# Kernel tuning notes

Hardware: AMD Instinct MI355X
Metric: run time of the kernel (lower is better)

## Reference

```python
import jax, jax.numpy as jnp
import numpy as np

R, B, D, C = 64, 4096, 512, 128  # n_rules, batch, n_fea, n_cls


def setup_inputs() -> dict:
    key = jax.random.key(0)
    k0, k1, k2, k3, k4 = jax.random.split(key, 5)
    x = jax.random.normal(k0, (B, D), dtype=jnp.float32)
    proto = jax.random.normal(k1, (R, D), dtype=jnp.float32)
    var = jax.random.uniform(k2, (R, D), dtype=jnp.float32)
    W = jax.random.normal(k3, (R, D, C), dtype=jnp.float32) * 0.02
    b = jax.random.normal(k4, (R, C), dtype=jnp.float32) * 0.02
    return {"x": x, "proto": proto, "var": var, "W": W, "b": b}


def reference(x, proto, var, W, b):
    # Antecedent: Gaussian membership per rule, var clamped to [1e-4, 0.1]
    v = jnp.clip(var, 0.0001, 0.1)                                  # [R, D]
    diff = x[None, :, :] - proto[:, None, :]                        # [R, B, D]
    m = jnp.exp(-diff * diff / (2.0 * v[:, None, :] ** 2))          # [R, B, D]
    # Firing strength: sum of squared memberships over features, softmax over rules
    fs_ini = jnp.sum(m * m, axis=-1).T                              # [B, R]
    fire_strength = jax.nn.softmax(fs_ini, axis=1)                  # [B, R]
    # Consequent: per-rule Linear + ReLU (batched GEMM over rules)
    expert = jax.nn.relu(jnp.einsum('bd,rdc->rbc', x, W) + b[:, None, :])  # [R, B, C]
    # Softmax-weighted combine over rules
    out = jnp.einsum('rbc,br->bc', expert, fire_strength)           # [B, C]
    return out, fire_strength
```

## Files before the change

### kernel.cpp

```cpp
#include <hip/hip_runtime.h>
#include <hip/hip_bf16.h>
#include <cmath>

#define R_ 64
#define B_ 4096
#define D_ 512
#define C_ 128

typedef __attribute__((ext_vector_type(8))) short bf16x8;
typedef __attribute__((ext_vector_type(4))) float f32x4;

__device__ __forceinline__ unsigned short f2bf(float f) {
  union { float f; unsigned u; } x; x.f = f;
  unsigned r = (x.u + 0x7FFFu + ((x.u >> 16) & 1u)) >> 16;
  return (unsigned short)r;
}

__global__ void prep_x_kernel(const float* __restrict__ x, unsigned short* __restrict__ xw) {
  int i = blockIdx.x * 256 + threadIdx.x;
  float4 v = reinterpret_cast<const float4*>(x)[i];
  ushort4 o;
  o.x = f2bf(v.x); o.y = f2bf(v.y); o.z = f2bf(v.z); o.w = f2bf(v.w);
  reinterpret_cast<ushort4*>(xw)[i] = o;
}

__global__ void prep_w_kernel(const float* __restrict__ W, unsigned short* __restrict__ wt) {
  __shared__ float t[32][33];
  int bx = blockIdx.x;
  int r = bx >> 6;
  int rem = bx & 63;
  int d0 = (rem >> 2) << 5;
  int c0 = (rem & 3) << 5;
  int tx = threadIdx.x & 31, ty = threadIdx.x >> 5;
  const float* Wr = W + (size_t)r * D_ * C_;
#pragma unroll
  for (int q = 0; q < 4; ++q) {
    int dl = q * 8 + ty;
    t[dl][tx] = Wr[(size_t)(d0 + dl) * C_ + c0 + tx];
  }
  __syncthreads();
  unsigned short* wtr = wt + (size_t)r * C_ * D_;
#pragma unroll
  for (int q = 0; q < 4; ++q) {
    int cl = q * 8 + ty;
    float v = t[tx][cl];
    wtr[(size_t)(c0 + cl) * D_ + d0 + tx] = f2bf(v);
  }
}

__global__ void prep_ps_kernel(const float* __restrict__ proto, const float* __restrict__ var,
                               float* __restrict__ ps) {
  int i = blockIdx.x * 256 + threadIdx.x;
  float v = fminf(fmaxf(var[i], 1e-4f), 0.1f);
  float s = 1.2011224087864498f / v;
  float2 o; o.x = s; o.y = -proto[i] * s;
  reinterpret_cast<float2*>(ps)[i] = o;
}

__global__ __launch_bounds__(256, 4) void fs_partial_kernel(
    const float* __restrict__ x, const float* __restrict__ ps,
    float* __restrict__ fire) {
  __shared__ float x_s[16 * 68];
  __shared__ __align__(16) float ps_s[64 * 128];
  const int tid = threadIdx.x;
  const int b0 = blockIdx.x * 16;
  const int dq = blockIdx.y;

  {
    int row = tid >> 4, c4 = tid & 15;
    float4 v = *reinterpret_cast<const float4*>(&x[(size_t)(b0 + row) * D_ + dq * 64 + c4 * 4]);
    *reinterpret_cast<float4*>(&x_s[row * 68 + c4 * 4]) = v;
  }
#pragma unroll
  for (int k = 0; k < 8; ++k) {
    int g = tid + k * 256;
    int row = g >> 5, gi = g & 31;
    float4 v = *reinterpret_cast<const float4*>(&ps[(size_t)row * (D_ * 2) + dq * 128 + gi * 4]);
    int gs = gi ^ (row & 31);
    *reinterpret_cast<float4*>((char*)ps_s + row * 512 + (gs << 4)) = v;
  }
  __syncthreads();

  const int tr = tid & 63;
  const int tb = tid >> 6;
  const int s31 = tr & 31;
  const char* pb = (const char*)ps_s + tr * 512;
  float facc[4] = {0.f, 0.f, 0.f, 0.f};

#pragma unroll
  for (int d4 = 0; d4 < 16; ++d4) {
    float4 psa = *reinterpret_cast<const float4*>(pb + ((((d4 * 2) ^ s31)) << 4));
    float4 psb = *reinterpret_cast<const float4*>(pb + ((((d4 * 2 + 1) ^ s31)) << 4));
#pragma unroll
    for (int i = 0; i < 4; ++i) {
      float4 xv = *reinterpret_cast<const float4*>(&x_s[(tb * 4 + i) * 68 + d4 * 4]);
      float u0 = fmaf(xv.x, psa.x, psa.y);
      float u1 = fmaf(xv.y, psa.z, psa.w);
      float u2 = fmaf(xv.z, psb.x, psb.y);
      float u3 = fmaf(xv.w, psb.z, psb.w);
      facc[i] += exp2f(-(u0 * u0)) + exp2f(-(u1 * u1)) +
                 exp2f(-(u2 * u2)) + exp2f(-(u3 * u3));
    }
  }
#pragma unroll
  for (int i = 0; i < 4; ++i)
    atomicAdd(&fire[(size_t)(b0 + tb * 4 + i) * R_ + tr], facc[i]);
}

__global__ void softmax_kernel(float* __restrict__ fire) {
  const int b = blockIdx.x * 4 + (threadIdx.x >> 6);
  const int r = threadIdx.x & 63;
  float v = fire[(size_t)b * R_ + r];
  float m = v;
#pragma unroll
  for (int off = 32; off; off >>= 1) m = fmaxf(m, __shfl_xor(m, off, 64));
  float e = exp2f((v - m) * 1.4426950408889634f);
  float s = e;
#pragma unroll
  for (int off = 32; off; off >>= 1) s += __shfl_xor(s, off, 64);
  fire[(size_t)b * R_ + r] = e / s;
}

__global__ __launch_bounds__(256, 2) void gemm_kernel(
    const unsigned short* __restrict__ xw, const unsigned short* __restrict__ wt,
    const float* __restrict__ fire, const float* __restrict__ bias,
    float* __restrict__ out) {
  __shared__ __align__(16) unsigned short x_s[2][128 * 64];
  __shared__ __align__(16) unsigned short w_s[2][128 * 64];
  __shared__ float fire_s[128 * 4];
  __shared__ float bias_s[4 * 128];

  const int tid = threadIdx.x;
  const int bm = blockIdx.x;
  const int rg = blockIdx.y;
  const int b0 = bm * 128;

  {
    for (int t = tid; t < 512; t += 256) {
      int row = t >> 2, g = t & 3;
      fire_s[t] = fire[(size_t)(b0 + row) * R_ + rg * 4 + g];
    }
    for (int t = tid; t < 512; t += 256) {
      bias_s[t] = bias[rg * 4 * C_ + t];
    }
  }

  const int wid = tid >> 6, lane = tid & 63;
  const int wm = wid >> 1, wn = wid & 1;
  const int l16 = lane & 15, lhi = lane >> 4;

  int offA[4][2], offB[4][2];
#pragma unroll
  for (int m = 0; m < 4; ++m) {
    int row = wm * 64 + m * 16 + l16;
#pragma unroll
    for (int ks = 0; ks < 2; ++ks)
      offA[m][ks] = row * 128 + (((ks * 4 + lhi) ^ (row & 7)) << 4);
  }
#pragma unroll
  for (int n = 0; n < 4; ++n) {
    int row = wn * 64 + n * 16 + l16;
#pragma unroll
    for (int ks = 0; ks < 2; ++ks)
      offB[n][ks] = row * 128 + (((ks * 4 + lhi) ^ (row & 7)) << 4);
  }

  const unsigned short* xsrc = xw + (size_t)b0 * D_;
  const unsigned short* wbase = wt + (size_t)(rg * 4) * C_ * D_;

  float tot[4][4][4];
#pragma unroll
  for (int m = 0; m < 4; ++m)
#pragma unroll
    for (int n = 0; n < 4; ++n)
#pragma unroll
      for (int j = 0; j < 4; ++j) tot[m][n][j] = 0.f;

  f32x4 acc[4][4];

  auto stage = [&](unsigned short* lds, const unsigned short* src, int kc) {
#pragma unroll
    for (int q = 0; q < 4; ++q) {
      int ch = q * 256 + tid;
      int row = ch >> 3, g = ch & 7;
      const unsigned short* ga = src + (size_t)row * D_ + kc + ((g ^ (row & 7)) << 3);
      __builtin_amdgcn_global_load_lds(
          (const __attribute__((address_space(1))) void*)ga,
          (__attribute__((address_space(3))) void*)(lds + ch * 8), 16, 0, 0);
    }
  };

  stage(x_s[0], xsrc, 0);
  stage(w_s[0], wbase, 0);
  asm volatile("s_waitcnt vmcnt(0)" ::: "memory");
  __syncthreads();

  int cur = 0;
  for (int s = 0; s < 32; ++s) {
    const int g = s >> 3, kk = s & 7;
    if (kk == 0) {
#pragma unroll
      for (int m = 0; m < 4; ++m)
#pragma unroll
        for (int n = 0; n < 4; ++n)
          acc[m][n] = f32x4{0.f, 0.f, 0.f, 0.f};
    }
    if (s + 1 < 32) {
      const int s1 = s + 1;
      stage(x_s[cur ^ 1], xsrc, (s1 & 7) * 64);
      stage(w_s[cur ^ 1], wbase + (size_t)(s1 >> 3) * C_ * D_, (s1 & 7) * 64);
    }
    const char* xb = (const char*)x_s[cur];
    const char* wb = (const char*)w_s[cur];
    bf16x8 av[4][2], bv[4][2];
#pragma unroll
    for (int m = 0; m < 4; ++m)
#pragma unroll
      for (int ks = 0; ks < 2; ++ks)
        av[m][ks] = *reinterpret_cast<const bf16x8*>(xb + offA[m][ks]);
#pragma unroll
    for (int n = 0; n < 4; ++n)
#pragma unroll
      for (int ks = 0; ks < 2; ++ks)
        bv[n][ks] = *reinterpret_cast<const bf16x8*>(wb + offB[n][ks]);
#pragma unroll
    for (int ks = 0; ks < 2; ++ks)
#pragma unroll
      for (int m = 0; m < 4; ++m)
#pragma unroll
        for (int n = 0; n < 4; ++n)
          acc[m][n] = __builtin_amdgcn_mfma_f32_16x16x32_bf16(av[m][ks], bv[n][ks], acc[m][n], 0, 0, 0);
    if (kk == 7) {
#pragma unroll
      for (int m = 0; m < 4; ++m)
#pragma unroll
        for (int n = 0; n < 4; ++n) {
          int col = wn * 64 + n * 16 + l16;
          float bi = bias_s[g * 128 + col];
#pragma unroll
          for (int j = 0; j < 4; ++j) {
            int rowl = wm * 64 + m * 16 + lhi * 4 + j;
            float v = acc[m][n][j] + bi;
            v = fmaxf(v, 0.f);
            tot[m][n][j] += v * fire_s[rowl * 4 + g];
          }
        }
    }
    asm volatile("s_waitcnt vmcnt(0)" ::: "memory");
    __syncthreads();
    cur ^= 1;
  }

#pragma unroll
  for (int m = 0; m < 4; ++m)
#pragma unroll
    for (int n = 0; n < 4; ++n) {
      int col = wn * 64 + n * 16 + l16;
#pragma unroll
      for (int j = 0; j < 4; ++j) {
        int rowl = wm * 64 + m * 16 + lhi * 4 + j;
        atomicAdd(&out[(size_t)(b0 + rowl) * C_ + col], tot[m][n][j]);
      }
    }
}

extern "C" void kernel_launch(void* const* d_in, const int* in_sizes, int n_in,
                              void* d_out, int out_size, void* d_ws, size_t ws_size,
                              hipStream_t stream) {
  const float* x     = (const float*)d_in[0];
  const float* proto = (const float*)d_in[1];
  const float* var   = (const float*)d_in[2];
  const float* W     = (const float*)d_in[3];
  const float* bias  = (const float*)d_in[4];
  float* out  = (float*)d_out;
  float* fire = out + (size_t)B_ * C_;

  const size_t WS_X  = (size_t)B_ * D_ * sizeof(unsigned short);
  const size_t WS_WT = (size_t)R_ * C_ * D_ * sizeof(unsigned short);
  const size_t WS_PS = (size_t)R_ * D_ * 2 * sizeof(float);
  if (ws_size < WS_X + WS_WT + WS_PS) return;

  unsigned short* xw  = (unsigned short*)d_ws;
  unsigned short* wtp = (unsigned short*)((char*)d_ws + WS_X);
  float*          ps  = (float*)((char*)d_ws + WS_X + WS_WT);

  hipMemsetAsync(d_out, 0, (size_t)out_size * sizeof(float), stream);
  prep_x_kernel<<<dim3((B_ * D_ / 4) / 256), dim3(256), 0, stream>>>(x, xw);
  prep_w_kernel<<<dim3(R_ * 64), dim3(256), 0, stream>>>(W, wtp);
  prep_ps_kernel<<<dim3(R_ * D_ / 256), dim3(256), 0, stream>>>(proto, var, ps);
  fs_partial_kernel<<<dim3(B_ / 16, 8), dim3(256), 0, stream>>>(x, ps, fire);
  softmax_kernel<<<dim3(B_ / 4), dim3(256), 0, stream>>>(fire);
  gemm_kernel<<<dim3(B_ / 128, R_ / 4), dim3(256), 0, stream>>>(xw, wtp, fire, bias, out);
}
```

Baseline: 121.3 us.

## Enlarge GEMM tile to 256x128 with 512 threads and triple-buffered prefetch

```diff
diff --git a/kernel.cpp b/kernel.cpp
--- a/kernel.cpp
+++ b/kernel.cpp
@@ -9,6 +9,8 @@
 
 typedef __attribute__((ext_vector_type(8))) short bf16x8;
 typedef __attribute__((ext_vector_type(4))) float f32x4;
+
+#define VMCNT(n) asm volatile("s_waitcnt vmcnt(" #n ")" ::: "memory")
 
 __device__ __forceinline__ unsigned short f2bf(float f) {
   union { float f; unsigned u; } x; x.f = f;
@@ -121,28 +123,28 @@
   fire[(size_t)b * R_ + r] = e / s;
 }
 
-__global__ __launch_bounds__(256, 2) void gemm_kernel(
+__global__ __launch_bounds__(512, 2) void gemm_kernel(
     const unsigned short* __restrict__ xw, const unsigned short* __restrict__ wt,
     const float* __restrict__ fire, const float* __restrict__ bias,
     float* __restrict__ out) {
-  __shared__ __align__(16) unsigned short x_s[2][128 * 64];
-  __shared__ __align__(16) unsigned short w_s[2][128 * 64];
-  __shared__ float fire_s[128 * 4];
+  __shared__ __align__(16) unsigned short x_s[3][256 * 64];
+  __shared__ __align__(16) unsigned short w_s[3][128 * 64];
+  __shared__ float fire_s[256 * 4];
   __shared__ float bias_s[4 * 128];
 
   const int tid = threadIdx.x;
-  const int bm = blockIdx.x;
-  const int rg = blockIdx.y;
-  const int b0 = bm * 128;
+  const int rg = blockIdx.x;
+  const int bm = blockIdx.y;
+  const int b0 = bm * 256;
 
   {
-    for (int t = tid; t < 512; t += 256) {
+#pragma unroll
+    for (int q = 0; q < 2; ++q) {
+      int t = q * 512 + tid;
       int row = t >> 2, g = t & 3;
       fire_s[t] = fire[(size_t)(b0 + row) * R_ + rg * 4 + g];
     }
-    for (int t = tid; t < 512; t += 256) {
-      bias_s[t] = bias[rg * 4 * C_ + t];
-    }
+    bias_s[tid >= 512 ? 0 : tid] = bias[rg * 4 * C_ + tid];
   }
 
   const int wid = tid >> 6, lane = tid & 63;
@@ -165,9 +167,40 @@
       offB[n][ks] = row * 128 + (((ks * 4 + lhi) ^ (row & 7)) << 4);
   }
 
+  int aoff[4], adst[4], boff[2], bdst[2];
+#pragma unroll
+  for (int q = 0; q < 4; ++q) {
+    int ch = q * 512 + tid;
+    int row = ch >> 3, g = ch & 7;
+    aoff[q] = row * D_ + ((g ^ (row & 7)) << 3);
+    adst[q] = ch * 8;
+  }
+#pragma unroll
+  for (int q = 0; q < 2; ++q) {
+    int ch = q * 512 + tid;
+    int row = ch >> 3, g = ch & 7;
+    boff[q] = row * D_ + ((g ^ (row & 7)) << 3);
+    bdst[q] = ch * 8;
+  }
+
   const unsigned short* xsrc = xw + (size_t)b0 * D_;
   const unsigned short* wbase = wt + (size_t)(rg * 4) * C_ * D_;
 
+  auto stageA = [&](unsigned short* lds, const unsigned short* src) {
+#pragma unroll
+    for (int q = 0; q < 4; ++q)
+      __builtin_amdgcn_global_load_lds(
+          (const __attribute__((address_space(1))) void*)(src + aoff[q]),
+          (__attribute__((address_space(3))) void*)(lds + adst[q]), 16, 0, 0);
+  };
+  auto stageB = [&](unsigned short* lds, const unsigned short* src) {
+#pragma unroll
+    for (int q = 0; q < 2; ++q)
+      __builtin_amdgcn_global_load_lds(
+          (const __attribute__((address_space(1))) void*)(src + boff[q]),
+          (__attribute__((address_space(3))) void*)(lds + bdst[q]), 16, 0, 0);
+  };
+
   float tot[4][4][4];
 #pragma unroll
   for (int m = 0; m < 4; ++m)
@@ -178,24 +211,13 @@
 
   f32x4 acc[4][4];
 
-  auto stage = [&](unsigned short* lds, const unsigned short* src, int kc) {
-#pragma unroll
-    for (int q = 0; q < 4; ++q) {
-      int ch = q * 256 + tid;
-      int row = ch >> 3, g = ch & 7;
-      const unsigned short* ga = src + (size_t)row * D_ + kc + ((g ^ (row & 7)) << 3);
-      __builtin_amdgcn_global_load_lds(
-          (const __attribute__((address_space(1))) void*)ga,
-          (__attribute__((address_space(3))) void*)(lds + ch * 8), 16, 0, 0);
-    }
-  };
-
-  stage(x_s[0], xsrc, 0);
-  stage(w_s[0], wbase, 0);
-  asm volatile("s_waitcnt vmcnt(0)" ::: "memory");
-  __syncthreads();
-
-  int cur = 0;
+  stageA(x_s[0], xsrc);
+  stageB(w_s[0], wbase);
+  stageA(x_s[1], xsrc + 64);
+  stageB(w_s[1], wbase + 64);
+  VMCNT(6);
+  __builtin_amdgcn_s_barrier();
+
   for (int s = 0; s < 32; ++s) {
     const int g = s >> 3, kk = s & 7;
     if (kk == 0) {
@@ -205,13 +227,15 @@
         for (int n = 0; n < 4; ++n)
           acc[m][n] = f32x4{0.f, 0.f, 0.f, 0.f};
     }
-    if (s + 1 < 32) {
-      const int s1 = s + 1;
-      stage(x_s[cur ^ 1], xsrc, (s1 & 7) * 64);
-      stage(w_s[cur ^ 1], wbase + (size_t)(s1 >> 3) * C_ * D_, (s1 & 7) * 64);
-    }
-    const char* xb = (const char*)x_s[cur];
-    const char* wb = (const char*)w_s[cur];
+    if (s + 2 < 32) {
+      const int s2 = s + 2;
+      unsigned short* xb2 = x_s[s2 % 3];
+      unsigned short* wb2 = w_s[s2 % 3];
+      stageA(xb2, xsrc + (s2 & 7) * 64);
+      stageB(wb2, wbase + (size_t)(s2 >> 3) * C_ * D_ + (s2 & 7) * 64);
+    }
+    const char* xb = (const char*)x_s[s % 3];
+    const char* wb = (const char*)w_s[s % 3];
     bf16x8 av[4][2], bv[4][2];
 #pragma unroll
     for (int m = 0; m < 4; ++m)
@@ -246,9 +270,9 @@
           }
         }
     }
-    asm volatile("s_waitcnt vmcnt(0)" ::: "memory");
-    __syncthreads();
-    cur ^= 1;
+    if (s < 30) { VMCNT(6); }
+    else if (s == 30) { VMCNT(0); }
+    if (s < 31) __builtin_amdgcn_s_barrier();
   }
 
 #pragma unroll
@@ -290,5 +314,5 @@
   prep_ps_kernel<<<dim3(R_ * D_ / 256), dim3(256), 0, stream>>>(proto, var, ps);
   fs_partial_kernel<<<dim3(B_ / 16, 8), dim3(256), 0, stream>>>(x, ps, fire);
   softmax_kernel<<<dim3(B_ / 4), dim3(256), 0, stream>>>(fire);
-  gemm_kernel<<<dim3(B_ / 128, R_ / 4), dim3(256), 0, stream>>>(xw, wtp, fire, bias, out);
-}
+  gemm_kernel<<<dim3(16, 16), dim3(512), 0, stream>>>(xw, wtp, fire, bias, out);
+}
```

Result: slower. 131.7 us (+8.6%).

## Shrink GEMM block tile, halve K step, and reorder grid for rule-major launch

Applied to the files above, without the earlier changes.

```diff
diff --git a/kernel.cpp b/kernel.cpp
--- a/kernel.cpp
+++ b/kernel.cpp
@@ -121,144 +121,146 @@
   fire[(size_t)b * R_ + r] = e / s;
 }
 
-__global__ __launch_bounds__(256, 2) void gemm_kernel(
+__global__ __launch_bounds__(256, 4) void gemm_kernel(
     const unsigned short* __restrict__ xw, const unsigned short* __restrict__ wt,
     const float* __restrict__ fire, const float* __restrict__ bias,
     float* __restrict__ out) {
-  __shared__ __align__(16) unsigned short x_s[2][128 * 64];
-  __shared__ __align__(16) unsigned short w_s[2][128 * 64];
-  __shared__ float fire_s[128 * 4];
+  __shared__ __align__(16) unsigned short x_s[2][64 * 32];
+  __shared__ __align__(16) unsigned short w_s[2][128 * 32];
+  __shared__ float fire_s[64 * 4];
   __shared__ float bias_s[4 * 128];
 
   const int tid = threadIdx.x;
-  const int bm = blockIdx.x;
-  const int rg = blockIdx.y;
-  const int b0 = bm * 128;
+  const int rg = blockIdx.x;
+  const int bm = blockIdx.y;
+  const int b0 = bm * 64;
 
   {
-    for (int t = tid; t < 512; t += 256) {
-      int row = t >> 2, g = t & 3;
-      fire_s[t] = fire[(size_t)(b0 + row) * R_ + rg * 4 + g];
-    }
-    for (int t = tid; t < 512; t += 256) {
-      bias_s[t] = bias[rg * 4 * C_ + t];
-    }
+    int row = tid >> 2, g = tid & 3;
+    fire_s[tid] = fire[(size_t)(b0 + row) * R_ + rg * 4 + g];
+    bias_s[tid] = bias[rg * 4 * C_ + tid];
+    bias_s[tid + 256] = bias[rg * 4 * C_ + tid + 256];
   }
 
   const int wid = tid >> 6, lane = tid & 63;
   const int wm = wid >> 1, wn = wid & 1;
   const int l16 = lane & 15, lhi = lane >> 4;
 
-  int offA[4][2], offB[4][2];
-#pragma unroll
-  for (int m = 0; m < 4; ++m) {
-    int row = wm * 64 + m * 16 + l16;
-#pragma unroll
-    for (int ks = 0; ks < 2; ++ks)
-      offA[m][ks] = row * 128 + (((ks * 4 + lhi) ^ (row & 7)) << 4);
+  int offA[2], offB[4];
+#pragma unroll
+  for (int m = 0; m < 2; ++m) {
+    int row = wm * 32 + m * 16 + l16;
+    offA[m] = row * 64 + ((lhi ^ (row & 3)) << 4);
   }
 #pragma unroll
   for (int n = 0; n < 4; ++n) {
     int row = wn * 64 + n * 16 + l16;
-#pragma unroll
-    for (int ks = 0; ks < 2; ++ks)
-      offB[n][ks] = row * 128 + (((ks * 4 + lhi) ^ (row & 7)) << 4);
+    offB[n] = row * 64 + ((lhi ^ (row & 3)) << 4);
+  }
+
+  int a_off, a_dst;
+  {
+    int ch = tid;
+    int row = ch >> 2, g4 = ch & 3;
+    a_off = row * D_ + ((g4 ^ (row & 3)) << 3);
+    a_dst = ch * 8;
+  }
+  int b_off[2], b_dst[2];
+#pragma unroll
+  for (int q = 0; q < 2; ++q) {
+    int ch = q * 256 + tid;
+    int row = ch >> 2, g4 = ch & 3;
+    b_off[q] = row * D_ + ((g4 ^ (row & 3)) << 3);
+    b_dst[q] = ch * 8;
   }
 
   const unsigned short* xsrc = xw + (size_t)b0 * D_;
   const unsigned short* wbase = wt + (size_t)(rg * 4) * C_ * D_;
 
-  float tot[4][4][4];
-#pragma unroll
-  for (int m = 0; m < 4; ++m)
+  auto stageA = [&](unsigned short* lds, int kc) {
+    __builtin_amdgcn_global_load_lds(
+        (const __attribute__((address_space(1))) void*)(xsrc + a_off + kc),
+        (__attribute__((address_space(3))) void*)(lds + a_dst), 16, 0, 0);
+  };
+  auto stageB = [&](unsigned short* lds, const unsigned short* src, int kc) {
+#pragma unroll
+    for (int q = 0; q < 2; ++q)
+      __builtin_amdgcn_global_load_lds(
+          (const __attribute__((address_space(1))) void*)(src + b_off[q] + kc),
+          (__attribute__((address_space(3))) void*)(lds + b_dst[q]), 16, 0, 0);
+  };
+
+  float tot[2][4][4];
+#pragma unroll
+  for (int m = 0; m < 2; ++m)
 #pragma unroll
     for (int n = 0; n < 4; ++n)
 #pragma unroll
       for (int j = 0; j < 4; ++j) tot[m][n][j] = 0.f;
 
-  f32x4 acc[4][4];
-
-  auto stage = [&](unsigned short* lds, const unsigned short* src, int kc) {
-#pragma unroll
-    for (int q = 0; q < 4; ++q) {
-      int ch = q * 256 + tid;
-      int row = ch >> 3, g = ch & 7;
-      const unsigned short* ga = src + (size_t)row * D_ + kc + ((g ^ (row & 7)) << 3);
-      __builtin_amdgcn_global_load_lds(
-          (const __attribute__((address_space(1))) void*)ga,
-          (__attribute__((address_space(3))) void*)(lds + ch * 8), 16, 0, 0);
-    }
-  };
-
-  stage(x_s[0], xsrc, 0);
-  stage(w_s[0], wbase, 0);
-  asm volatile("s_waitcnt vmcnt(0)" ::: "memory");
+  f32x4 acc[2][4];
+
+  stageA(x_s[0], 0);
+  stageB(w_s[0], wbase, 0);
   __syncthreads();
 
   int cur = 0;
-  for (int s = 0; s < 32; ++s) {
-    const int g = s >> 3, kk = s & 7;
+  for (int s = 0; s < 64; ++s) {
+    const int g = s >> 4, kk = s & 15;
     if (kk == 0) {
 #pragma unroll
-      for (int m = 0; m < 4; ++m)
+      for (int m = 0; m < 2; ++m)
 #pragma unroll
         for (int n = 0; n < 4; ++n)
           acc[m][n] = f32x4{0.f, 0.f, 0.f, 0.f};
     }
-    if (s + 1 < 32) {
+    if (s + 1 < 64) {
       const int s1 = s + 1;
-      stage(x_s[cur ^ 1], xsrc, (s1 & 7) * 64);
-      stage(w_s[cur ^ 1], wbase + (size_t)(s1 >> 3) * C_ * D_, (s1 & 7) * 64);
+      stageA(x_s[cur ^ 1], (s1 & 15) * 32);
+      stageB(w_s[cur ^ 1], wbase + (size_t)(s1 >> 4) * C_ * D_, (s1 & 15) * 32);
     }
     const char* xb = (const char*)x_s[cur];
     const char* wb = (const char*)w_s[cur];
-    bf16x8 av[4][2], bv[4][2];
-#pragma unroll
-    for (int m = 0; m < 4; ++m)
-#pragma unroll
-      for (int ks = 0; ks < 2; ++ks)
-        av[m][ks] = *reinterpret_cast<const bf16x8*>(xb + offA[m][ks]);
+    bf16x8 av[2], bv[4];
+#pragma unroll
+    for (int m = 0; m < 2; ++m)
+      av[m] = *reinterpret_cast<const bf16x8*>(xb + offA[m]);
 #pragma unroll
     for (int n = 0; n < 4; ++n)
-#pragma unroll
-      for (int ks = 0; ks < 2; ++ks)
-        bv[n][ks] = *reinterpret_cast<const bf16x8*>(wb + offB[n][ks]);
-#pragma unroll
-    for (int ks = 0; ks < 2; ++ks)
-#pragma unroll
-      for (int m = 0; m < 4; ++m)
-#pragma unroll
-        for (int n = 0; n < 4; ++n)
-          acc[m][n] = __builtin_amdgcn_mfma_f32_16x16x32_bf16(av[m][ks], bv[n][ks], acc[m][n], 0, 0, 0);
-    if (kk == 7) {
-#pragma unroll
-      for (int m = 0; m < 4; ++m)
+      bv[n] = *reinterpret_cast<const bf16x8*>(wb + offB[n]);
+#pragma unroll
+    for (int m = 0; m < 2; ++m)
+#pragma unroll
+      for (int n = 0; n < 4; ++n)
+        acc[m][n] = __builtin_amdgcn_mfma_f32_16x16x32_bf16(av[m], bv[n], acc[m][n], 0, 0, 0);
+    if (kk == 15) {
+#pragma unroll
+      for (int m = 0; m < 2; ++m)
 #pragma unroll
         for (int n = 0; n < 4; ++n) {
           int col = wn * 64 + n * 16 + l16;
           float bi = bias_s[g * 128 + col];
 #pragma unroll
           for (int j = 0; j < 4; ++j) {
-            int rowl = wm * 64 + m * 16 + lhi * 4 + j;
+            int rowl = wm * 32 + m * 16 + lhi * 4 + j;
             float v = acc[m][n][j] + bi;
             v = fmaxf(v, 0.f);
             tot[m][n][j] += v * fire_s[rowl * 4 + g];
           }
         }
     }
-    asm volatile("s_waitcnt vmcnt(0)" ::: "memory");
     __syncthreads();
     cur ^= 1;
   }
 
 #pragma unroll
-  for (int m = 0; m < 4; ++m)
+  for (int m = 0; m < 2; ++m)
 #pragma unroll
     for (int n = 0; n < 4; ++n) {
       int col = wn * 64 + n * 16 + l16;
 #pragma unroll
       for (int j = 0; j < 4; ++j) {
-        int rowl = wm * 64 + m * 16 + lhi * 4 + j;
+        int rowl = wm * 32 + m * 16 + lhi * 4 + j;
         atomicAdd(&out[(size_t)(b0 + rowl) * C_ + col], tot[m][n][j]);
       }
     }
@@ -290,5 +292,5 @@
   prep_ps_kernel<<<dim3(R_ * D_ / 256), dim3(256), 0, stream>>>(proto, var, ps);
   fs_partial_kernel<<<dim3(B_ / 16, 8), dim3(256), 0, stream>>>(x, ps, fire);
   softmax_kernel<<<dim3(B_ / 4), dim3(256), 0, stream>>>(fire);
-  gemm_kernel<<<dim3(B_ / 128, R_ / 4), dim3(256), 0, stream>>>(xw, wtp, fire, bias, out);
-}
+  gemm_kernel<<<dim3(16, 64), dim3(256), 0, stream>>>(xw, wtp, fire, bias, out);
+}
```

New measurement: 129.3 us (median of 3 runs). 1.07x slower.

## Pre-pack x and W into MFMA fragment layout and drop LDS staging in GEMM

Applied to the files above, without the earlier changes.

```diff
diff --git a/kernel.cpp b/kernel.cpp
--- a/kernel.cpp
+++ b/kernel.cpp
@@ -16,35 +16,56 @@
   return (unsigned short)r;
 }
 
-__global__ void prep_x_kernel(const float* __restrict__ x, unsigned short* __restrict__ xw) {
-  int i = blockIdx.x * 256 + threadIdx.x;
-  float4 v = reinterpret_cast<const float4*>(x)[i];
-  ushort4 o;
-  o.x = f2bf(v.x); o.y = f2bf(v.y); o.z = f2bf(v.z); o.w = f2bf(v.w);
-  reinterpret_cast<ushort4*>(xw)[i] = o;
-}
-
-__global__ void prep_w_kernel(const float* __restrict__ W, unsigned short* __restrict__ wt) {
-  __shared__ float t[32][33];
-  int bx = blockIdx.x;
-  int r = bx >> 6;
-  int rem = bx & 63;
-  int d0 = (rem >> 2) << 5;
-  int c0 = (rem & 3) << 5;
-  int tx = threadIdx.x & 31, ty = threadIdx.x >> 5;
-  const float* Wr = W + (size_t)r * D_ * C_;
-#pragma unroll
-  for (int q = 0; q < 4; ++q) {
-    int dl = q * 8 + ty;
-    t[dl][tx] = Wr[(size_t)(d0 + dl) * C_ + c0 + tx];
+__global__ __launch_bounds__(256) void prep_xf_kernel(const float* __restrict__ x,
+                                                      unsigned short* __restrict__ xf) {
+  __shared__ float s[16][516];
+  const int mt = blockIdx.x;
+  const int t = threadIdx.x;
+#pragma unroll
+  for (int p = 0; p < 8; ++p) {
+    int idx = p * 256 + t;
+    int row = idx >> 7, c4 = idx & 127;
+    float4 v = *reinterpret_cast<const float4*>(&x[(size_t)(mt * 16 + row) * D_ + c4 * 4]);
+    *reinterpret_cast<float4*>(&s[row][c4 * 4]) = v;
   }
   __syncthreads();
-  unsigned short* wtr = wt + (size_t)r * C_ * D_;
-#pragma unroll
-  for (int q = 0; q < 4; ++q) {
-    int cl = q * 8 + ty;
-    float v = t[tx][cl];
-    wtr[(size_t)(c0 + cl) * D_ + d0 + tx] = f2bf(v);
+  const int lane = t & 63, l16 = lane & 15, lhi = lane >> 4;
+#pragma unroll
+  for (int p = 0; p < 4; ++p) {
+    int kc = (t >> 6) + p * 4;
+    const float* src = &s[l16][kc * 32 + lhi * 8];
+    unsigned short o[8];
+#pragma unroll
+    for (int e = 0; e < 8; ++e) o[e] = f2bf(src[e]);
+    *reinterpret_cast<bf16x8*>(xf + ((size_t)(mt * 16 + kc)) * 512 + lane * 8) =
+        *reinterpret_cast<bf16x8*>(o);
+  }
+}
+
+__global__ __launch_bounds__(256) void prep_wf_kernel(const float* __restrict__ W,
+                                                      unsigned short* __restrict__ wf) {
+  __shared__ float s[32][132];
+  const int kc = blockIdx.x;
+  const int r = blockIdx.y;
+  const int t = threadIdx.x;
+#pragma unroll
+  for (int p = 0; p < 4; ++p) {
+    int idx = p * 256 + t;
+    int row = idx >> 5, c4 = idx & 31;
+    float4 v = *reinterpret_cast<const float4*>(
+        &W[((size_t)r * D_ + kc * 32 + row) * C_ + c4 * 4]);
+    *reinterpret_cast<float4*>(&s[row][c4 * 4]) = v;
+  }
+  __syncthreads();
+  const int lane = t & 63, l16 = lane & 15, lhi = lane >> 4;
+#pragma unroll
+  for (int p = 0; p < 2; ++p) {
+    int nt = (t >> 6) + p * 4;
+    unsigned short o[8];
+#pragma unroll
+    for (int e = 0; e < 8; ++e) o[e] = f2bf(s[lhi * 8 + e][nt * 16 + l16]);
+    *reinterpret_cast<bf16x8*>(wf + ((size_t)((r * 8 + nt) * 16 + kc)) * 512 + lane * 8) =
+        *reinterpret_cast<bf16x8*>(o);
   }
 }
 
@@ -122,51 +143,29 @@
 }
 
 __global__ __launch_bounds__(256, 2) void gemm_kernel(
-    const unsigned short* __restrict__ xw, const unsigned short* __restrict__ wt,
+    const unsigned short* __restrict__ xf, const unsigned short* __restrict__ wf,
     const float* __restrict__ fire, const float* __restrict__ bias,
     float* __restrict__ out) {
-  __shared__ __align__(16) unsigned short x_s[2][128 * 64];
-  __shared__ __align__(16) unsigned short w_s[2][128 * 64];
-  __shared__ float fire_s[128 * 4];
-  __shared__ float bias_s[4 * 128];
-
   const int tid = threadIdx.x;
   const int bm = blockIdx.x;
   const int rg = blockIdx.y;
   const int b0 = bm * 128;
 
-  {
-    for (int t = tid; t < 512; t += 256) {
-      int row = t >> 2, g = t & 3;
-      fire_s[t] = fire[(size_t)(b0 + row) * R_ + rg * 4 + g];
-    }
-    for (int t = tid; t < 512; t += 256) {
-      bias_s[t] = bias[rg * 4 * C_ + t];
-    }
-  }
-
   const int wid = tid >> 6, lane = tid & 63;
   const int wm = wid >> 1, wn = wid & 1;
   const int l16 = lane & 15, lhi = lane >> 4;
 
-  int offA[4][2], offB[4][2];
-#pragma unroll
-  for (int m = 0; m < 4; ++m) {
-    int row = wm * 64 + m * 16 + l16;
-#pragma unroll
-    for (int ks = 0; ks < 2; ++ks)
-      offA[m][ks] = row * 128 + (((ks * 4 + lhi) ^ (row & 7)) << 4);
-  }
-#pragma unroll
-  for (int n = 0; n < 4; ++n) {
-    int row = wn * 64 + n * 16 + l16;
-#pragma unroll
-    for (int ks = 0; ks < 2; ++ks)
-      offB[n][ks] = row * 128 + (((ks * 4 + lhi) ^ (row & 7)) << 4);
-  }
-
-  const unsigned short* xsrc = xw + (size_t)b0 * D_;
-  const unsigned short* wbase = wt + (size_t)(rg * 4) * C_ * D_;
+  const unsigned short* abase[4];
+#pragma unroll
+  for (int m = 0; m < 4; ++m)
+    abase[m] = xf + ((size_t)((bm * 8 + wm * 4 + m) * 16)) * 512 + lane * 8;
+
+  float bias_r[4][4];
+#pragma unroll
+  for (int g = 0; g < 4; ++g)
+#pragma unroll
+    for (int n = 0; n < 4; ++n)
+      bias_r[g][n] = bias[(rg * 4 + g) * C_ + wn * 64 + n * 16 + l16];
 
   float tot[4][4][4];
 #pragma unroll
@@ -176,79 +175,58 @@
 #pragma unroll
       for (int j = 0; j < 4; ++j) tot[m][n][j] = 0.f;
 
-  f32x4 acc[4][4];
-
-  auto stage = [&](unsigned short* lds, const unsigned short* src, int kc) {
-#pragma unroll
-    for (int q = 0; q < 4; ++q) {
-      int ch = q * 256 + tid;
-      int row = ch >> 3, g = ch & 7;
-      const unsigned short* ga = src + (size_t)row * D_ + kc + ((g ^ (row & 7)) << 3);
-      __builtin_amdgcn_global_load_lds(
-          (const __attribute__((address_space(1))) void*)ga,
-          (__attribute__((address_space(3))) void*)(lds + ch * 8), 16, 0, 0);
-    }
-  };
-
-  stage(x_s[0], xsrc, 0);
-  stage(w_s[0], wbase, 0);
-  asm volatile("s_waitcnt vmcnt(0)" ::: "memory");
-  __syncthreads();
-
-  int cur = 0;
-  for (int s = 0; s < 32; ++s) {
-    const int g = s >> 3, kk = s & 7;
-    if (kk == 0) {
+  for (int g = 0; g < 4; ++g) {
+    const unsigned short* bbase[4];
+#pragma unroll
+    for (int n = 0; n < 4; ++n)
+      bbase[n] = wf + ((size_t)(((rg * 4 + g) * 8 + wn * 4 + n) * 16)) * 512 + lane * 8;
+
+    f32x4 acc[4][4];
+#pragma unroll
+    for (int m = 0; m < 4; ++m)
+#pragma unroll
+      for (int n = 0; n < 4; ++n)
+        acc[m][n] = f32x4{0.f, 0.f, 0.f, 0.f};
+
+    bf16x8 av[2][4], bv[2][4];
+#pragma unroll
+    for (int m = 0; m < 4; ++m) av[0][m] = *reinterpret_cast<const bf16x8*>(abase[m]);
+#pragma unroll
+    for (int n = 0; n < 4; ++n) bv[0][n] = *reinterpret_cast<const bf16x8*>(bbase[n]);
+
+#pragma unroll
+    for (int kc = 0; kc < 16; ++kc) {
+      const int cur = kc & 1, nxt = cur ^ 1;
+      if (kc < 15) {
+#pragma unroll
+        for (int m = 0; m < 4; ++m)
+          av[nxt][m] = *reinterpret_cast<const bf16x8*>(abase[m] + (kc + 1) * 512);
+#pragma unroll
+        for (int n = 0; n < 4; ++n)
+          bv[nxt][n] = *reinterpret_cast<const bf16x8*>(bbase[n] + (kc + 1) * 512);
+      }
 #pragma unroll
       for (int m = 0; m < 4; ++m)
 #pragma unroll
         for (int n = 0; n < 4; ++n)
-          acc[m][n] = f32x4{0.f, 0.f, 0.f, 0.f};
-    }
-    if (s + 1 < 32) {
-      const int s1 = s + 1;
-      stage(x_s[cur ^ 1], xsrc, (s1 & 7) * 64);
-      stage(w_s[cur ^ 1], wbase + (size_t)(s1 >> 3) * C_ * D_, (s1 & 7) * 64);
-    }
-    const char* xb = (const char*)x_s[cur];
-    const char* wb = (const char*)w_s[cur];
-    bf16x8 av[4][2], bv[4][2];
-#pragma unroll
-    for (int m = 0; m < 4; ++m)
-#pragma unroll
-      for (int ks = 0; ks < 2; ++ks)
-        av[m][ks] = *reinterpret_cast<const bf16x8*>(xb + offA[m][ks]);
-#pragma unroll
-    for (int n = 0; n < 4; ++n)
-#pragma unroll
-      for (int ks = 0; ks < 2; ++ks)
-        bv[n][ks] = *reinterpret_cast<const bf16x8*>(wb + offB[n][ks]);
-#pragma unroll
-    for (int ks = 0; ks < 2; ++ks)
-#pragma unroll
-      for (int m = 0; m < 4; ++m)
-#pragma unroll
-        for (int n = 0; n < 4; ++n)
-          acc[m][n] = __builtin_amdgcn_mfma_f32_16x16x32_bf16(av[m][ks], bv[n][ks], acc[m][n], 0, 0, 0);
-    if (kk == 7) {
-#pragma unroll
-      for (int m = 0; m < 4; ++m)
-#pragma unroll
-        for (int n = 0; n < 4; ++n) {
-          int col = wn * 64 + n * 16 + l16;
-          float bi = bias_s[g * 128 + col];
-#pragma unroll
-          for (int j = 0; j < 4; ++j) {
-            int rowl = wm * 64 + m * 16 + lhi * 4 + j;
-            float v = acc[m][n][j] + bi;
-            v = fmaxf(v, 0.f);
-            tot[m][n][j] += v * fire_s[rowl * 4 + g];
-          }
+          acc[m][n] = __builtin_amdgcn_mfma_f32_16x16x32_bf16(av[cur][m], bv[cur][n], acc[m][n], 0, 0, 0);
+    }
+
+#pragma unroll
+    for (int m = 0; m < 4; ++m) {
+      float fire_v[4];
+#pragma unroll
+      for (int j = 0; j < 4; ++j)
+        fire_v[j] = fire[(size_t)(b0 + wm * 64 + m * 16 + lhi * 4 + j) * R_ + rg * 4 + g];
+#pragma unroll
+      for (int n = 0; n < 4; ++n)
+#pragma unroll
+        for (int j = 0; j < 4; ++j) {
+          float v = acc[m][n][j] + bias_r[g][n];
+          v = fmaxf(v, 0.f);
+          tot[m][n][j] += v * fire_v[j];
         }
     }
-    asm volatile("s_waitcnt vmcnt(0)" ::: "memory");
-    __syncthreads();
-    cur ^= 1;
   }
 
 #pragma unroll
@@ -275,20 +253,20 @@
   float* out  = (float*)d_out;
   float* fire = out + (size_t)B_ * C_;
 
-  const size_t WS_X  = (size_t)B_ * D_ * sizeof(unsigned short);
-  const size_t WS_WT = (size_t)R_ * C_ * D_ * sizeof(unsigned short);
+  const size_t WS_XF = (size_t)B_ * D_ * sizeof(unsigned short);
+  const size_t WS_WF = (size_t)R_ * C_ * D_ * sizeof(unsigned short);
   const size_t WS_PS = (size_t)R_ * D_ * 2 * sizeof(float);
-  if (ws_size < WS_X + WS_WT + WS_PS) return;
-
-  unsigned short* xw  = (unsigned short*)d_ws;
-  unsigned short* wtp = (unsigned short*)((char*)d_ws + WS_X);
-  float*          ps  = (float*)((char*)d_ws + WS_X + WS_WT);
+  if (ws_size < WS_XF + WS_WF + WS_PS) return;
+
+  unsigned short* xf = (unsigned short*)d_ws;
+  unsigned short* wfp = (unsigned short*)((char*)d_ws + WS_XF);
+  float*          ps  = (float*)((char*)d_ws + WS_XF + WS_WF);
 
   hipMemsetAsync(d_out, 0, (size_t)out_size * sizeof(float), stream);
-  prep_x_kernel<<<dim3((B_ * D_ / 4) / 256), dim3(256), 0, stream>>>(x, xw);
-  prep_w_kernel<<<dim3(R_ * 64), dim3(256), 0, stream>>>(W, wtp);
+  prep_xf_kernel<<<dim3(B_ / 16), dim3(256), 0, stream>>>(x, xf);
+  prep_wf_kernel<<<dim3(16, 64), dim3(256), 0, stream>>>(W, wfp);
   prep_ps_kernel<<<dim3(R_ * D_ / 256), dim3(256), 0, stream>>>(proto, var, ps);
   fs_partial_kernel<<<dim3(B_ / 16, 8), dim3(256), 0, stream>>>(x, ps, fire);
   softmax_kernel<<<dim3(B_ / 4), dim3(256), 0, stream>>>(fire);
-  gemm_kernel<<<dim3(B_ / 128, R_ / 4), dim3(256), 0, stream>>>(xw, wtp, fire, bias, out);
-}
+  gemm_kernel<<<dim3(B_ / 128, R_ / 4), dim3(256), 0, stream>>>(xf, wfp, fire, bias, out);
+}
```

Measured after the change: 337.2 us. +178.0%, slower.
